# Kernel optimization log

Hardware: AMD Instinct MI355X
Metric: run time of the kernel (lower is better)

## Reference

```python
import jax, jax.numpy as jnp
import numpy as np

KNN_K = 16
EPS = 1e-5


def _knn_idx(p, k):
    # p: [B,3,N] -> idx [B,N,k] of nearest neighbors (self excluded)
    pt = jnp.swapaxes(p, 1, 2)                      # [B,N,3]
    xx = jnp.sum(pt * pt, axis=-1)                  # [B,N]
    inner = jnp.einsum('bnd,bmd->bnm', pt, pt)      # [B,N,N]
    dist = -(xx[:, :, None] - 2.0 * inner + xx[:, None, :])  # -||pi-pj||^2
    N = pt.shape[1]
    dist = dist - 1e9 * jnp.eye(N, dtype=dist.dtype)
    return jax.lax.top_k(dist, k)[1]


def _ln(x, g, b):
    mu = jnp.mean(x, axis=-1, keepdims=True)
    var = jnp.mean((x - mu) ** 2, axis=-1, keepdims=True)
    return (x - mu) * jax.lax.rsqrt(var + EPS) * g + b


_gather = jax.vmap(lambda a, i: a[i])  # a:[N,C], i:[N,k] -> [N,k,C]


def setup_inputs() -> dict:
    key = jax.random.key(0)
    ks = jax.random.split(key, 24)
    Cin, C, B, N = 64, 128, 8, 2048
    s = lambda k_, shp, fan: jax.random.normal(k_, shp, jnp.float32) * (1.0 / np.sqrt(fan))
    return {
        'x': jax.random.normal(ks[0], (B, Cin, N), jnp.float32),
        'p': jax.random.normal(ks[1], (B, 3, N), jnp.float32),
        'Win': s(ks[2], (C, Cin), Cin), 'bin_': jnp.zeros((C,), jnp.float32),
        'Wq': s(ks[3], (C, C), C), 'Wk': s(ks[4], (C, C), C), 'Wv': s(ks[5], (C, C), C),
        'Wd1': s(ks[6], (C, 3), 3), 'bd1': jnp.zeros((C,), jnp.float32),
        'Wd2': s(ks[7], (C, C), C), 'bd2': jnp.zeros((C,), jnp.float32),
        'Wa': s(ks[8], (C, C), C), 'ba': jnp.zeros((C,), jnp.float32),
        'g1': jnp.ones((C,), jnp.float32), 'b1': jnp.zeros((C,), jnp.float32),
        'g2': jnp.ones((C,), jnp.float32), 'b2': jnp.zeros((C,), jnp.float32),
        'Wf1': s(ks[9], (4 * C, C), C), 'bf1': jnp.zeros((4 * C,), jnp.float32),
        'Wf2': s(ks[10], (C, 4 * C), 4 * C), 'bf2': jnp.zeros((C,), jnp.float32),
    }


def reference(x, p, Win, bin_, Wq, Wk, Wv, Wd1, bd1, Wd2, bd2, Wa, ba,
              g1, b1, g2, b2, Wf1, bf1, Wf2, bf2) -> jnp.ndarray:
    B, _, N = x.shape
    k = min(KNN_K, max(1, N - 1))
    # in_proj (conv1x1 == per-point linear); work in [B,N,C]
    h = jnp.einsum('oc,bcn->bno', Win, x) + bin_          # [B,N,C]
    hn = _ln(h, g1, b1)
    idx = _knn_idx(p, k)                                  # [B,N,k] (int)
    q = hn @ Wq.T                                         # [B,N,C]
    k_all = hn @ Wk.T
    v_all = hn @ Wv.T
    k_j = _gather(k_all, idx)                             # [B,N,k,C]
    v_j = _gather(v_all, idx)
    pt = jnp.swapaxes(p, 1, 2)                            # [B,N,3]
    p_j = _gather(pt, idx)                                # [B,N,k,3]
    rel = pt[:, :, None, :] - p_j                         # [B,N,k,3]
    d = jax.nn.relu(rel @ Wd1.T + bd1) @ Wd2.T + bd2      # [B,N,k,C]
    logits = (q[:, :, None, :] - k_j + d) @ Wa.T + ba     # [B,N,k,C]
    a = jax.nn.softmax(logits, axis=2)                    # softmax over neighbors
    y = jnp.sum(a * (v_j + d), axis=2)                    # [B,N,C]
    h = h + y
    h2 = _ln(h, g2, b2)
    h = h + jax.nn.relu(h2 @ Wf1.T + bf1) @ Wf2.T + bf2
    return jnp.swapaxes(h, 1, 2)                          # [B,C,N]
```

## Files before the change

### kernel.cpp

```cpp
#include <hip/hip_runtime.h>

typedef __bf16 bf16_t;
typedef __bf16 bf16x8 __attribute__((ext_vector_type(8)));
typedef __bf16 bf16x2 __attribute__((ext_vector_type(2)));
typedef float  f32x4  __attribute__((ext_vector_type(4)));

#define MFMA16(a,b,c) __builtin_amdgcn_mfma_f32_16x16x32_bf16((a),(b),(c),0,0,0)

#define BB 8
#define NN 2048
#define CC 128
#define CIN 64
#define KNB 16
#define BNT (BB*NN)

static __device__ __forceinline__ int remap256(int x) { return ((x & 7) << 5) | (x >> 3); }

static __device__ __forceinline__ bf16x8 cvt8(const float* src) {
  f32x4 a0 = *(const f32x4*)src;
  f32x4 a1 = *(const f32x4*)(src + 4);
  bf16x8 fr;
  fr[0] = (__bf16)a0[0]; fr[1] = (__bf16)a0[1]; fr[2] = (__bf16)a0[2]; fr[3] = (__bf16)a0[3];
  fr[4] = (__bf16)a1[0]; fr[5] = (__bf16)a1[1]; fr[6] = (__bf16)a1[2]; fr[7] = (__bf16)a1[3];
  return fr;
}

__global__ __launch_bounds__(256) void inproj_compw_k(
    const float* __restrict__ x, const float* __restrict__ Win, const float* __restrict__ bin,
    const float* __restrict__ g1, const float* __restrict__ b1,
    bf16_t* __restrict__ hb, bf16_t* __restrict__ hnb,
    const float* __restrict__ Wq, const float* __restrict__ Wk, const float* __restrict__ Wv,
    const float* __restrict__ Wd2, const float* __restrict__ Wa,
    const float* __restrict__ Wf1, const float* __restrict__ Wf2,
    bf16_t* __restrict__ Wqb, bf16_t* __restrict__ Wkb, bf16_t* __restrict__ Wvb,
    bf16_t* __restrict__ Wd2b, bf16_t* __restrict__ Wab,
    bf16_t* __restrict__ Wf1b, bf16_t* __restrict__ Wf2b) {
  __shared__ bf16_t As[64 * 72];
  __shared__ bf16_t Bs[128 * 72];
  __shared__ float hs[64 * 132];
  int t = threadIdx.x;
  if (blockIdx.x >= 256) {
    int bi = blockIdx.x - 256;
    int mat = bi >> 3, xi = bi & 7;
    int nel = (mat >= 5) ? 65536 : 16384;
    const float* S = mat == 0 ? Wq : mat == 1 ? Wk : mat == 2 ? Wv : mat == 3 ? Wd2
                   : mat == 4 ? Wa : mat == 5 ? Wf1 : Wf2;
    bf16_t* D = mat == 0 ? Wqb : mat == 1 ? Wkb : mat == 2 ? Wvb : mat == 3 ? Wd2b
              : mat == 4 ? Wab : mat == 5 ? Wf1b : Wf2b;
    for (int i = xi * 256 + t; i * 8 < nel; i += 2048)
      *(bf16x8*)(D + i * 8) = cvt8(S + i * 8);
    return;
  }
  int lane = t & 63, w = t >> 6, quad = lane >> 4, l15 = lane & 15;
  int mBase = remap256(blockIdx.x) * 64;
  int b = mBase >> 11, n0 = mBase & (NN - 1);
  const float* xb = x + (size_t)b * CIN * NN;
  {
    int k = t >> 2, part = t & 3;
    #pragma unroll
    for (int i = 0; i < 4; ++i) {
      f32x4 v = *(const f32x4*)(xb + (size_t)k * NN + n0 + part * 16 + i * 4);
      #pragma unroll
      for (int j2 = 0; j2 < 4; ++j2) As[(part * 16 + i * 4 + j2) * 72 + k] = (__bf16)v[j2];
    }
  }
  {
    int row = t >> 1, seg = (t & 1) * 32;
    #pragma unroll
    for (int i = 0; i < 4; ++i)
      *(bf16x8*)(&Bs[row * 72 + seg + i * 8]) = cvt8(Win + (size_t)row * CIN + seg + i * 8);
  }
  __syncthreads();
  f32x4 acc[2][4] = {};
  #pragma unroll
  for (int s = 0; s < 2; ++s) {
    bf16x8 af[4];
    #pragma unroll
    for (int mt = 0; mt < 4; ++mt)
      af[mt] = *(const bf16x8*)(&As[(mt * 16 + l15) * 72 + s * 32 + quad * 8]);
    #pragma unroll
    for (int t2 = 0; t2 < 2; ++t2) {
      bf16x8 bfr = *(const bf16x8*)(&Bs[((w * 2 + t2) * 16 + l15) * 72 + s * 32 + quad * 8]);
      #pragma unroll
      for (int mt = 0; mt < 4; ++mt) acc[t2][mt] = MFMA16(af[mt], bfr, acc[t2][mt]);
    }
  }
  #pragma unroll
  for (int t2 = 0; t2 < 2; ++t2) {
    int col = (w * 2 + t2) * 16 + l15;
    float bv = bin[col];
    #pragma unroll
    for (int mt = 0; mt < 4; ++mt)
      #pragma unroll
      for (int reg = 0; reg < 4; ++reg)
        hs[(mt * 16 + quad * 4 + reg) * 132 + col] = acc[t2][mt][reg] + bv;
  }
  __syncthreads();
  {
    int row = t >> 2, c0 = (t & 3) * 32;
    float v[32];
    #pragma unroll
    for (int i = 0; i < 8; ++i) *(f32x4*)(v + i * 4) = *(const f32x4*)(&hs[row * 132 + c0 + i * 4]);
    float s1 = 0.f, s2 = 0.f;
    #pragma unroll
    for (int i = 0; i < 32; ++i) { s1 += v[i]; s2 += v[i] * v[i]; }
    s1 += __shfl_xor(s1, 1); s1 += __shfl_xor(s1, 2);
    s2 += __shfl_xor(s2, 1); s2 += __shfl_xor(s2, 2);
    float mu = s1 * (1.f / CC);
    float var = s2 * (1.f / CC) - mu * mu;
    float rs = rsqrtf(var + 1e-5f);
    bf16_t* hrow = hb + (size_t)(mBase + row) * CC + c0;
    #pragma unroll
    for (int i = 0; i < 4; ++i) {
      bf16x8 ho;
      #pragma unroll
      for (int j = 0; j < 8; ++j) ho[j] = (__bf16)v[i * 8 + j];
      *(bf16x8*)(hrow + i * 8) = ho;
    }
    bf16_t* hnrow = hnb + (size_t)(mBase + row) * CC + c0;
    #pragma unroll
    for (int i = 0; i < 4; ++i) {
      f32x4 g4a = ((const f32x4*)g1)[(c0 >> 2) + i * 2],     g4b = ((const f32x4*)g1)[(c0 >> 2) + i * 2 + 1];
      f32x4 b4a = ((const f32x4*)b1)[(c0 >> 2) + i * 2],     b4b = ((const f32x4*)b1)[(c0 >> 2) + i * 2 + 1];
      bf16x8 o;
      #pragma unroll
      for (int j = 0; j < 4; ++j) o[j]     = (__bf16)((v[i * 8 + j]     - mu) * rs * g4a[j] + b4a[j]);
      #pragma unroll
      for (int j = 0; j < 4; ++j) o[4 + j] = (__bf16)((v[i * 8 + 4 + j] - mu) * rs * g4b[j] + b4b[j]);
      *(bf16x8*)(hnrow + i * 8) = o;
    }
  }
}

static __device__ __forceinline__ void cas(double& a, double& b) {
  double lo = fmin(a, b), hi = fmax(a, b); a = lo; b = hi;
}
#define S8(K,o) \
  cas(K[o+0],K[o+1]); cas(K[o+2],K[o+3]); cas(K[o+4],K[o+5]); cas(K[o+6],K[o+7]); \
  cas(K[o+0],K[o+2]); cas(K[o+1],K[o+3]); cas(K[o+4],K[o+6]); cas(K[o+5],K[o+7]); \
  cas(K[o+1],K[o+2]); cas(K[o+5],K[o+6]); \
  cas(K[o+0],K[o+4]); cas(K[o+1],K[o+5]); cas(K[o+2],K[o+6]); cas(K[o+3],K[o+7]); \
  cas(K[o+2],K[o+4]); cas(K[o+3],K[o+5]); \
  cas(K[o+1],K[o+2]); cas(K[o+3],K[o+4]); cas(K[o+5],K[o+6]);
#define M8(K,a,b) \
  K[a+0]=fmin(K[a+0],K[b+7]); K[a+1]=fmin(K[a+1],K[b+6]); K[a+2]=fmin(K[a+2],K[b+5]); K[a+3]=fmin(K[a+3],K[b+4]); \
  K[a+4]=fmin(K[a+4],K[b+3]); K[a+5]=fmin(K[a+5],K[b+2]); K[a+6]=fmin(K[a+6],K[b+1]); K[a+7]=fmin(K[a+7],K[b+0]); \
  cas(K[a+0],K[a+4]); cas(K[a+1],K[a+5]); cas(K[a+2],K[a+6]); cas(K[a+3],K[a+7]); \
  cas(K[a+0],K[a+2]); cas(K[a+1],K[a+3]); cas(K[a+4],K[a+6]); cas(K[a+5],K[a+7]); \
  cas(K[a+0],K[a+1]); cas(K[a+2],K[a+3]); cas(K[a+4],K[a+5]); cas(K[a+6],K[a+7]);

static __device__ void knn_impl(float* sp, const float* __restrict__ p,
                                int* __restrict__ idxo, int bid) {
  float* px = sp; float* py = sp + NN; float* pz = sp + 2 * NN;
  int t = threadIdx.x;
  int b = bid >> 9;
  int g = bid & 511;
  const float* pb = p + (size_t)b * 3 * NN;
  for (int i = t; i < NN; i += 256) { px[i] = pb[i]; py[i] = pb[NN + i]; pz[i] = pb[2 * NN + i]; }
  __syncthreads();
  int w = t >> 6, lane = t & 63;
  int n = g * 4 + w;
  float pnx = px[n], pny = py[n], pnz = pz[n];
  double key[32];
  #pragma unroll
  for (int s = 0; s < 32; ++s) {
    int m = s * 64 + lane;
    float dx = pnx - px[m], dy = pny - py[m], dz = pnz - pz[m];
    float dist = dx * dx + dy * dy + dz * dz;
    unsigned db = (m == n) ? 0x7F800000u : __float_as_uint(dist);
    key[s] = __hiloint2double((int)db, m);
  }
  S8(key, 0); S8(key, 8); S8(key, 16); S8(key, 24);
  M8(key, 0, 8); M8(key, 16, 24); M8(key, 0, 16);
  const double DINF = __hiloint2double(0x7F900000, 0);
  int* myout = idxo + ((size_t)b * NN + n) * KNB;
  #pragma unroll 1
  for (int r = 0; r < 16; ++r) {
    double gm = key[0];
    #pragma unroll
    for (int off = 1; off < 64; off <<= 1) {
      double o = __shfl_xor(gm, off);
      gm = fmin(gm, o);
    }
    if (lane == 0) myout[r] = __double2loint(gm);
    bool win = (key[0] == gm);
    key[0] = win ? key[1] : key[0];
    key[1] = win ? key[2] : key[1];
    key[2] = win ? key[3] : key[2];
    key[3] = win ? key[4] : key[3];
    key[4] = win ? key[5] : key[4];
    key[5] = win ? key[6] : key[5];
    key[6] = win ? key[7] : key[6];
    key[7] = win ? DINF   : key[7];
  }
}

template<int EPI>
static __device__ void gemm_body(bf16_t* As, bf16_t* Bs,
    const bf16_t* __restrict__ Ab, const bf16_t* __restrict__ Wb, const float* __restrict__ bias,
    float* __restrict__ outF, bf16_t* __restrict__ outB, const bf16_t* __restrict__ resid,
    int mBase, int nBase, int Ncol, int Kdim) {
  int t = threadIdx.x;
  int lane = t & 63, w = t >> 6, quad = lane >> 4, l15 = lane & 15;
  int r = t >> 2, seg = (t & 3) * 8;
  f32x4 acc[4] = {{0,0,0,0},{0,0,0,0},{0,0,0,0},{0,0,0,0}};
  for (int k0 = 0; k0 < Kdim; k0 += 32) {
    __syncthreads();
    *(bf16x8*)(&As[r * 40 + seg]) = *(const bf16x8*)(Ab + (size_t)(mBase + r) * Kdim + k0 + seg);
    *(bf16x8*)(&Bs[r * 40 + seg]) = *(const bf16x8*)(Wb + (size_t)(nBase + r) * Kdim + k0 + seg);
    __syncthreads();
    bf16x8 bfr = *(const bf16x8*)(&Bs[(w * 16 + l15) * 40 + quad * 8]);
    #pragma unroll
    for (int mt = 0; mt < 4; ++mt) {
      bf16x8 afr = *(const bf16x8*)(&As[(mt * 16 + l15) * 40 + quad * 8]);
      acc[mt] = MFMA16(afr, bfr, acc[mt]);
    }
  }
  int n = nBase + w * 16 + l15;
  float bv = bias ? bias[n] : 0.f;
  #pragma unroll
  for (int mt = 0; mt < 4; ++mt) {
    #pragma unroll
    for (int reg = 0; reg < 4; ++reg) {
      int m = mBase + mt * 16 + quad * 4 + reg;
      float val = acc[mt][reg] + bv;
      if (EPI == 1) {
        outB[(size_t)m * Ncol + n] = (__bf16)fmaxf(val, 0.f);
      } else if (EPI == 3) {
        outB[(size_t)m * Ncol + n] = (__bf16)val;
      } else {
        val += (float)resid[(size_t)m * CC + n];
        int bo = m >> 11, np = m & (NN - 1);
        outF[((size_t)bo * CC + n) * NN + np] = val;
      }
    }
  }
}

template<int EPI>
__global__ __launch_bounds__(256) void gemm_k(
    const bf16_t* __restrict__ Ab, const bf16_t* __restrict__ Wb, const float* __restrict__ bias,
    float* __restrict__ outF, bf16_t* __restrict__ outB, const bf16_t* __restrict__ resid,
    int Ncol, int Kdim) {
  __shared__ bf16_t As[64 * 40];
  __shared__ bf16_t Bs[64 * 40];
  gemm_body<EPI>(As, Bs, Ab, Wb, bias, outF, outB, resid,
                 remap256(blockIdx.x) * 64, blockIdx.y * 64, Ncol, Kdim);
}

__global__ __launch_bounds__(256) void knn_qkv_k(
    const float* __restrict__ p, int* __restrict__ idxo,
    const bf16_t* __restrict__ hnb,
    const bf16_t* __restrict__ Wqb, const bf16_t* __restrict__ Wkb, const bf16_t* __restrict__ Wvb,
    bf16_t* __restrict__ qb, bf16_t* __restrict__ kb, bf16_t* __restrict__ vb) {
  __shared__ __align__(16) char smem[3 * NN * 4];
  if (blockIdx.x < 4096) {
    knn_impl((float*)smem, p, idxo, blockIdx.x);
  } else {
    bf16_t* As = (bf16_t*)smem;
    bf16_t* Bs = As + 64 * 40;
    int bx = blockIdx.x - 4096;
    int yy = bx >> 8, xx = bx & 255;
    int sel = yy >> 1;
    int mB = remap256(xx) * 64, nB = (yy & 1) * 64;
    if (sel == 0)      gemm_body<3>(As, Bs, hnb, Wqb, nullptr, nullptr, qb, nullptr, mB, nB, CC, CC);
    else if (sel == 1) gemm_body<3>(As, Bs, hnb, Wkb, nullptr, nullptr, kb, nullptr, mB, nB, CC, CC);
    else               gemm_body<3>(As, Bs, hnb, Wvb, nullptr, nullptr, vb, nullptr, mB, nB, CC, CC);
  }
}

__global__ __launch_bounds__(256, 3) void attn_k(
    const bf16_t* __restrict__ qbuf, const bf16_t* __restrict__ kbuf, const bf16_t* __restrict__ vbuf,
    const float* __restrict__ p, const int* __restrict__ idx,
    const float* __restrict__ Wd1, const float* __restrict__ bd1,
    const bf16_t* __restrict__ Wd2b, const float* __restrict__ bd2,
    const bf16_t* __restrict__ Wab, const float* __restrict__ ba,
    const float* __restrict__ g2, const float* __restrict__ b2,
    const bf16_t* __restrict__ hb, bf16_t* __restrict__ hresb, bf16_t* __restrict__ h2) {
  __shared__ bf16_t ts[64 * 136];
  __shared__ float hrs[4 * 128];
  __shared__ f32x4 wd1s[128];
  __shared__ f32x4 rels4[64];
  __shared__ int idxs[64];
  int t = threadIdx.x;
  int lane = t & 63, w = t >> 6, quad = lane >> 4, l15 = lane & 15;
  int batch = blockIdx.x & 7, grp = blockIdx.x >> 3;
  int bn0 = batch * NN + grp * 4;
  int b = batch;
  const float* pb = p + (size_t)b * 3 * NN;
  int col0 = w * 32 + l15;
  int col1 = col0 + 16;

  bf16x8 Bd[2][4];
  #pragma unroll
  for (int t2 = 0; t2 < 2; ++t2) {
    int row = w * 32 + t2 * 16 + l15;
    #pragma unroll
    for (int s = 0; s < 4; ++s)
      Bd[t2][s] = *(const bf16x8*)(Wd2b + (size_t)row * CC + s * 32 + quad * 8);
  }

  if (t < 64) {
    int jj = idx[(size_t)bn0 * KNB + t];
    idxs[t] = jj;
    int npt = grp * 4 + (t >> 4);
    f32x4 rv;
    rv[0] = pb[npt]          - pb[jj];
    rv[1] = pb[NN + npt]     - pb[NN + jj];
    rv[2] = pb[2 * NN + npt] - pb[2 * NN + jj];
    rv[3] = 0.f;
    rels4[t] = rv;
  }
  if (t < 128) {
    f32x4 wv;
    wv[0] = Wd1[t * 3]; wv[1] = Wd1[t * 3 + 1]; wv[2] = Wd1[t * 3 + 2]; wv[3] = bd1[t];
    wd1s[t] = wv;
  }
  __syncthreads();

  float qv[2][4];
  #pragma unroll
  for (int mt = 0; mt < 4; ++mt) {
    qv[0][mt] = (float)qbuf[(size_t)(bn0 + mt) * CC + col0];
    qv[1][mt] = (float)qbuf[(size_t)(bn0 + mt) * CC + col1];
  }
  float kreg[2][4][4];
  #pragma unroll
  for (int mt = 0; mt < 4; ++mt)
    #pragma unroll
    for (int reg = 0; reg < 4; ++reg) {
      size_t base = (size_t)(b * NN + idxs[mt * 16 + quad * 4 + reg]) * CC;
      kreg[0][mt][reg] = (float)kbuf[base + col0];
      kreg[1][mt][reg] = (float)kbuf[base + col1];
    }

  f32x4 relv[4];
  #pragma unroll
  for (int mt = 0; mt < 4; ++mt) relv[mt] = rels4[mt * 16 + l15];
  f32x4 accd[2][4] = {};
  #pragma unroll
  for (int s = 0; s < 4; ++s) {
    bf16x8 af[4];
    #pragma unroll
    for (int j = 0; j < 8; ++j) {
      f32x4 wv = wd1s[s * 32 + quad * 8 + j];
      #pragma unroll
      for (int mt = 0; mt < 4; ++mt) {
        float tv = fmaf(wv[0], relv[mt][0], fmaf(wv[1], relv[mt][1], fmaf(wv[2], relv[mt][2], wv[3])));
        af[mt][j] = (__bf16)fmaxf(tv, 0.f);
      }
    }
    #pragma unroll
    for (int t2 = 0; t2 < 2; ++t2)
      #pragma unroll
      for (int mt = 0; mt < 4; ++mt)
        accd[t2][mt] = MFMA16(af[mt], Bd[t2][s], accd[t2][mt]);
  }

  {
    float b2v0 = bd2[col0], b2v1 = bd2[col1];
    #pragma unroll
    for (int mt = 0; mt < 4; ++mt)
      #pragma unroll
      for (int reg = 0; reg < 4; ++reg) {
        int row = mt * 16 + quad * 4 + reg;
        float d0 = accd[0][mt][reg] + b2v0;
        float d1 = accd[1][mt][reg] + b2v1;
        accd[0][mt][reg] = d0;
        accd[1][mt][reg] = d1;
        ts[row * 136 + col0] = (__bf16)(qv[0][mt] - kreg[0][mt][reg] + d0);
        ts[row * 136 + col1] = (__bf16)(qv[1][mt] - kreg[1][mt][reg] + d1);
      }
  }
  __syncthreads();

  float vreg[2][4][4];
  #pragma unroll
  for (int mt = 0; mt < 4; ++mt)
    #pragma unroll
    for (int reg = 0; reg < 4; ++reg) {
      size_t base = (size_t)(b * NN + idxs[mt * 16 + quad * 4 + reg]) * CC;
      vreg[0][mt][reg] = (float)vbuf[base + col0];
      vreg[1][mt][reg] = (float)vbuf[base + col1];
    }
  float hv[2][4];
  if (quad == 0) {
    #pragma unroll
    for (int mt = 0; mt < 4; ++mt) {
      hv[0][mt] = (float)hb[(size_t)(bn0 + mt) * CC + col0];
      hv[1][mt] = (float)hb[(size_t)(bn0 + mt) * CC + col1];
    }
  }
  bf16x8 Ba[2][4];
  #pragma unroll
  for (int t2 = 0; t2 < 2; ++t2) {
    int row = w * 32 + t2 * 16 + l15;
    #pragma unroll
    for (int s = 0; s < 4; ++s)
      Ba[t2][s] = *(const bf16x8*)(Wab + (size_t)row * CC + s * 32 + quad * 8);
  }

  f32x4 accl[2][4] = {};
  #pragma unroll
  for (int s = 0; s < 4; ++s) {
    bf16x8 af[4];
    #pragma unroll
    for (int mt = 0; mt < 4; ++mt)
      af[mt] = *(const bf16x8*)(&ts[(mt * 16 + l15) * 136 + s * 32 + quad * 8]);
    #pragma unroll
    for (int t2 = 0; t2 < 2; ++t2)
      #pragma unroll
      for (int mt = 0; mt < 4; ++mt)
        accl[t2][mt] = MFMA16(af[mt], Ba[t2][s], accl[t2][mt]);
  }

  #pragma unroll
  for (int t2 = 0; t2 < 2; ++t2) {
    int col = t2 ? col1 : col0;
    float bav = ba[col];
    #pragma unroll
    for (int mt = 0; mt < 4; ++mt) {
      float lv0 = accl[t2][mt][0] + bav, lv1 = accl[t2][mt][1] + bav;
      float lv2 = accl[t2][mt][2] + bav, lv3 = accl[t2][mt][3] + bav;
      float mx = fmaxf(fmaxf(lv0, lv1), fmaxf(lv2, lv3));
      mx = fmaxf(mx, __shfl_xor(mx, 16));
      mx = fmaxf(mx, __shfl_xor(mx, 32));
      float e0 = __expf(lv0 - mx), e1 = __expf(lv1 - mx);
      float e2 = __expf(lv2 - mx), e3 = __expf(lv3 - mx);
      float ss = e0 + e1 + e2 + e3;
      ss += __shfl_xor(ss, 16); ss += __shfl_xor(ss, 32);
      float yv = e0 * (vreg[t2][mt][0] + accd[t2][mt][0])
               + e1 * (vreg[t2][mt][1] + accd[t2][mt][1])
               + e2 * (vreg[t2][mt][2] + accd[t2][mt][2])
               + e3 * (vreg[t2][mt][3] + accd[t2][mt][3]);
      yv += __shfl_xor(yv, 16); yv += __shfl_xor(yv, 32);
      if (quad == 0) {
        float hvv = hv[t2][mt] + yv / ss;
        hresb[(size_t)(bn0 + mt) * CC + col] = (__bf16)hvv;
        hrs[mt * 128 + col] = hvv;
      }
    }
  }
  __syncthreads();

  {
    int c0 = lane * 2;
    float v0 = hrs[w * 128 + c0], v1 = hrs[w * 128 + c0 + 1];
    float s1 = v0 + v1, s2 = v0 * v0 + v1 * v1;
    #pragma unroll
    for (int off = 1; off < 64; off <<= 1) { s1 += __shfl_xor(s1, off); s2 += __shfl_xor(s2, off); }
    float mu = s1 * (1.f / CC);
    float var = s2 * (1.f / CC) - mu * mu;
    float rs = rsqrtf(var + 1e-5f);
    bf16x2 o;
    o[0] = (__bf16)((v0 - mu) * rs * g2[c0] + b2[c0]);
    o[1] = (__bf16)((v1 - mu) * rs * g2[c0 + 1] + b2[c0 + 1]);
    *(bf16x2*)(h2 + (size_t)(bn0 + w) * CC + c0) = o;
  }
}

extern "C" void kernel_launch(void* const* d_in, const int* in_sizes, int n_in,
                              void* d_out, int out_size, void* d_ws, size_t ws_size,
                              hipStream_t stream) {
  const float* x   = (const float*)d_in[0];
  const float* p   = (const float*)d_in[1];
  const float* Win = (const float*)d_in[2];
  const float* bin = (const float*)d_in[3];
  const float* Wq  = (const float*)d_in[4];
  const float* Wk  = (const float*)d_in[5];
  const float* Wv  = (const float*)d_in[6];
  const float* Wd1 = (const float*)d_in[7];
  const float* bd1 = (const float*)d_in[8];
  const float* Wd2 = (const float*)d_in[9];
  const float* bd2 = (const float*)d_in[10];
  const float* Wa  = (const float*)d_in[11];
  const float* ba  = (const float*)d_in[12];
  const float* g1  = (const float*)d_in[13];
  const float* b1  = (const float*)d_in[14];
  const float* g2  = (const float*)d_in[15];
  const float* b2  = (const float*)d_in[16];
  const float* Wf1 = (const float*)d_in[17];
  const float* bf1 = (const float*)d_in[18];
  const float* Wf2 = (const float*)d_in[19];
  const float* bf2 = (const float*)d_in[20];
  float* out = (float*)d_out;

  const size_t SZ = (size_t)BNT * CC;
  float* wsf = (float*)d_ws;
  bf16_t* hb    = (bf16_t*)wsf;
  bf16_t* hnb   = (bf16_t*)(wsf + SZ / 2);
  bf16_t* hresb = hnb;
  bf16_t* qb    = (bf16_t*)(wsf + SZ);
  bf16_t* kb    = (bf16_t*)(wsf + SZ + SZ / 2);
  bf16_t* vb    = (bf16_t*)(wsf + 2 * SZ);
  bf16_t* g     = (bf16_t*)(wsf + SZ);
  bf16_t* h2    = (bf16_t*)(wsf + 3 * SZ);
  int*    idxw  = (int*)(wsf + 3 * SZ + SZ / 2);
  bf16_t* Wqb   = (bf16_t*)(idxw + (size_t)BNT * KNB);
  bf16_t* Wkb   = Wqb  + 16384;
  bf16_t* Wvb   = Wkb  + 16384;
  bf16_t* Wd2b  = Wvb  + 16384;
  bf16_t* Wab   = Wd2b + 16384;
  bf16_t* Wf1b  = Wab  + 16384;
  bf16_t* Wf2b  = Wf1b + 65536;

  inproj_compw_k<<<256 + 56, 256, 0, stream>>>(x, Win, bin, g1, b1, hb, hnb,
                                               Wq, Wk, Wv, Wd2, Wa, Wf1, Wf2,
                                               Wqb, Wkb, Wvb, Wd2b, Wab, Wf1b, Wf2b);
  knn_qkv_k<<<4096 + 1536, 256, 0, stream>>>(p, idxw, hnb, Wqb, Wkb, Wvb, qb, kb, vb);
  attn_k<<<BNT / 4, 256, 0, stream>>>(qb, kb, vb, p, idxw, Wd1, bd1, Wd2b, bd2, Wab, ba,
                                      g2, b2, hb, hresb, h2);
  gemm_k<1><<<dim3(BNT / 64, 8), 256, 0, stream>>>(h2, Wf1b, bf1, nullptr, g, nullptr, 4 * CC, CC);
  gemm_k<2><<<dim3(BNT / 64, 2), 256, 0, stream>>>(g, Wf2b, bf2, out, nullptr, hresb, CC, 4 * CC);
}
```

Baseline: 255.5 us.

## Fold Wa into Wq, Wk and Wd2 to drop the per-neighbor logits GEMM

Uses the linearity of the logits projection to precompute Wa·Wq, Wa·Wk and Wa·Wd2 (plus Wa·bd2) as combined weights. The q/k projections now produce Wa-projected values directly, and the attention kernel computes logits from the relu(Wd1·rel) tile with a single MFMA pass against Wa·Wd2. This removes the second dependent GEMM and its LDS round trip. The cost is a small extra weight-product precompute and different bf16 rounding, since the logits skip the intermediate rounding step.

After: 260.7 us. 2.1% more time.

```diff
diff --git a/kernel.cpp b/kernel.cpp
--- a/kernel.cpp
+++ b/kernel.cpp
@@ -2,6 +2,7 @@
 
 typedef __bf16 bf16_t;
 typedef __bf16 bf16x8 __attribute__((ext_vector_type(8)));
+typedef __bf16 bf16x4 __attribute__((ext_vector_type(4)));
 typedef __bf16 bf16x2 __attribute__((ext_vector_type(2)));
 typedef float  f32x4  __attribute__((ext_vector_type(4)));
 
@@ -31,24 +32,53 @@
     bf16_t* __restrict__ hb, bf16_t* __restrict__ hnb,
     const float* __restrict__ Wq, const float* __restrict__ Wk, const float* __restrict__ Wv,
     const float* __restrict__ Wd2, const float* __restrict__ Wa,
-    const float* __restrict__ Wf1, const float* __restrict__ Wf2,
-    bf16_t* __restrict__ Wqb, bf16_t* __restrict__ Wkb, bf16_t* __restrict__ Wvb,
-    bf16_t* __restrict__ Wd2b, bf16_t* __restrict__ Wab,
-    bf16_t* __restrict__ Wf1b, bf16_t* __restrict__ Wf2b) {
+    const float* __restrict__ Wf1, const float* __restrict__ Wf2, const float* __restrict__ bd2,
+    bf16_t* __restrict__ Wqab, bf16_t* __restrict__ Wkab, bf16_t* __restrict__ Wvb,
+    bf16_t* __restrict__ Wd2b, bf16_t* __restrict__ Wd2ab,
+    bf16_t* __restrict__ Wf1b, bf16_t* __restrict__ Wf2b, float* __restrict__ bd2a) {
   __shared__ bf16_t As[64 * 72];
   __shared__ bf16_t Bs[128 * 72];
   __shared__ float hs[64 * 132];
   int t = threadIdx.x;
   if (blockIdx.x >= 256) {
     int bi = blockIdx.x - 256;
-    int mat = bi >> 3, xi = bi & 7;
-    int nel = (mat >= 5) ? 65536 : 16384;
-    const float* S = mat == 0 ? Wq : mat == 1 ? Wk : mat == 2 ? Wv : mat == 3 ? Wd2
-                   : mat == 4 ? Wa : mat == 5 ? Wf1 : Wf2;
-    bf16_t* D = mat == 0 ? Wqb : mat == 1 ? Wkb : mat == 2 ? Wvb : mat == 3 ? Wd2b
-              : mat == 4 ? Wab : mat == 5 ? Wf1b : Wf2b;
-    for (int i = xi * 256 + t; i * 8 < nel; i += 2048)
-      *(bf16x8*)(D + i * 8) = cvt8(S + i * 8);
+    if (bi < 32) {
+      int mat = bi >> 3, xi = bi & 7;
+      int nel = (mat >= 2) ? 65536 : 16384;
+      const float* S = mat == 0 ? Wv : mat == 1 ? Wd2 : mat == 2 ? Wf1 : Wf2;
+      bf16_t* D = mat == 0 ? Wvb : mat == 1 ? Wd2b : mat == 2 ? Wf1b : Wf2b;
+      for (int i = xi * 256 + t; i * 8 < nel; i += 2048)
+        *(bf16x8*)(D + i * 8) = cvt8(S + i * 8);
+    } else if (bi < 80) {
+      int pi = bi - 32, mat = pi >> 4, xi = pi & 15;
+      const float* R = mat == 0 ? Wq : mat == 1 ? Wk : Wd2;
+      bf16_t* D = mat == 0 ? Wqab : mat == 1 ? Wkab : Wd2ab;
+      int c = xi * 8 + (t >> 5);
+      int i0 = (t & 31) * 4;
+      const float* war = Wa + (size_t)c * CC;
+      f32x4 acc = {0.f, 0.f, 0.f, 0.f};
+      #pragma unroll 4
+      for (int e = 0; e < CC; ++e) {
+        float a = war[e];
+        f32x4 bq = *(const f32x4*)(R + (size_t)e * CC + i0);
+        acc[0] = fmaf(a, bq[0], acc[0]);
+        acc[1] = fmaf(a, bq[1], acc[1]);
+        acc[2] = fmaf(a, bq[2], acc[2]);
+        acc[3] = fmaf(a, bq[3], acc[3]);
+      }
+      bf16x4 o;
+      o[0] = (__bf16)acc[0]; o[1] = (__bf16)acc[1];
+      o[2] = (__bf16)acc[2]; o[3] = (__bf16)acc[3];
+      *(bf16x4*)(D + (size_t)c * CC + i0) = o;
+    } else {
+      if (t < 128) {
+        float s = 0.f;
+        const float* war = Wa + (size_t)t * CC;
+        #pragma unroll 4
+        for (int e = 0; e < CC; ++e) s = fmaf(war[e], bd2[e], s);
+        bd2a[t] = s;
+      }
+    }
     return;
   }
   int lane = t & 63, w = t >> 6, quad = lane >> 4, l15 = lane & 15;
@@ -251,7 +281,7 @@
 __global__ __launch_bounds__(256) void knn_qkv_k(
     const float* __restrict__ p, int* __restrict__ idxo,
     const bf16_t* __restrict__ hnb,
-    const bf16_t* __restrict__ Wqb, const bf16_t* __restrict__ Wkb, const bf16_t* __restrict__ Wvb,
+    const bf16_t* __restrict__ Wqab, const bf16_t* __restrict__ Wkab, const bf16_t* __restrict__ Wvb,
     bf16_t* __restrict__ qb, bf16_t* __restrict__ kb, bf16_t* __restrict__ vb) {
   __shared__ __align__(16) char smem[3 * NN * 4];
   if (blockIdx.x < 4096) {
@@ -263,8 +293,8 @@
     int yy = bx >> 8, xx = bx & 255;
     int sel = yy >> 1;
     int mB = remap256(xx) * 64, nB = (yy & 1) * 64;
-    if (sel == 0)      gemm_body<3>(As, Bs, hnb, Wqb, nullptr, nullptr, qb, nullptr, mB, nB, CC, CC);
-    else if (sel == 1) gemm_body<3>(As, Bs, hnb, Wkb, nullptr, nullptr, kb, nullptr, mB, nB, CC, CC);
+    if (sel == 0)      gemm_body<3>(As, Bs, hnb, Wqab, nullptr, nullptr, qb, nullptr, mB, nB, CC, CC);
+    else if (sel == 1) gemm_body<3>(As, Bs, hnb, Wkab, nullptr, nullptr, kb, nullptr, mB, nB, CC, CC);
     else               gemm_body<3>(As, Bs, hnb, Wvb, nullptr, nullptr, vb, nullptr, mB, nB, CC, CC);
   }
 }
@@ -274,7 +304,8 @@
     const float* __restrict__ p, const int* __restrict__ idx,
     const float* __restrict__ Wd1, const float* __restrict__ bd1,
     const bf16_t* __restrict__ Wd2b, const float* __restrict__ bd2,
-    const bf16_t* __restrict__ Wab, const float* __restrict__ ba,
+    const bf16_t* __restrict__ Wd2ab, const float* __restrict__ bd2a,
+    const float* __restrict__ ba,
     const float* __restrict__ g2, const float* __restrict__ b2,
     const bf16_t* __restrict__ hb, bf16_t* __restrict__ hresb, bf16_t* __restrict__ h2) {
   __shared__ bf16_t ts[64 * 136];
@@ -286,19 +317,9 @@
   int lane = t & 63, w = t >> 6, quad = lane >> 4, l15 = lane & 15;
   int batch = blockIdx.x & 7, grp = blockIdx.x >> 3;
   int bn0 = batch * NN + grp * 4;
-  int b = batch;
-  const float* pb = p + (size_t)b * 3 * NN;
+  const float* pb = p + (size_t)batch * 3 * NN;
   int col0 = w * 32 + l15;
   int col1 = col0 + 16;
-
-  bf16x8 Bd[2][4];
-  #pragma unroll
-  for (int t2 = 0; t2 < 2; ++t2) {
-    int row = w * 32 + t2 * 16 + l15;
-    #pragma unroll
-    for (int s = 0; s < 4; ++s)
-      Bd[t2][s] = *(const bf16x8*)(Wd2b + (size_t)row * CC + s * 32 + quad * 8);
-  }
 
   if (t < 64) {
     int jj = idx[(size_t)bn0 * KNB + t];
@@ -318,68 +339,105 @@
   }
   __syncthreads();
 
-  float qv[2][4];
-  #pragma unroll
-  for (int mt = 0; mt < 4; ++mt) {
-    qv[0][mt] = (float)qbuf[(size_t)(bn0 + mt) * CC + col0];
-    qv[1][mt] = (float)qbuf[(size_t)(bn0 + mt) * CC + col1];
-  }
-  float kreg[2][4][4];
-  #pragma unroll
-  for (int mt = 0; mt < 4; ++mt)
-    #pragma unroll
-    for (int reg = 0; reg < 4; ++reg) {
-      size_t base = (size_t)(b * NN + idxs[mt * 16 + quad * 4 + reg]) * CC;
-      kreg[0][mt][reg] = (float)kbuf[base + col0];
-      kreg[1][mt][reg] = (float)kbuf[base + col1];
-    }
-
-  f32x4 relv[4];
-  #pragma unroll
-  for (int mt = 0; mt < 4; ++mt) relv[mt] = rels4[mt * 16 + l15];
+  {
+    int row = t >> 2, cseg = (t & 3) * 32;
+    f32x4 rv = rels4[row];
+    #pragma unroll
+    for (int i = 0; i < 4; ++i) {
+      bf16x8 u8;
+      #pragma unroll
+      for (int j = 0; j < 8; ++j) {
+        f32x4 wv = wd1s[cseg + i * 8 + j];
+        float tv = fmaf(wv[0], rv[0], fmaf(wv[1], rv[1], fmaf(wv[2], rv[2], wv[3])));
+        u8[j] = (__bf16)fmaxf(tv, 0.f);
+      }
+      *(bf16x8*)(&ts[row * 136 + cseg + i * 8]) = u8;
+    }
+  }
+  __syncthreads();
+
+  f32x4 acca[2][4] = {};
+  {
+    bf16x8 Bf[2][4];
+    #pragma unroll
+    for (int t2 = 0; t2 < 2; ++t2) {
+      int row = w * 32 + t2 * 16 + l15;
+      #pragma unroll
+      for (int s = 0; s < 4; ++s)
+        Bf[t2][s] = *(const bf16x8*)(Wd2ab + (size_t)row * CC + s * 32 + quad * 8);
+    }
+    #pragma unroll
+    for (int s = 0; s < 4; ++s) {
+      bf16x8 af[4];
+      #pragma unroll
+      for (int mt = 0; mt < 4; ++mt)
+        af[mt] = *(const bf16x8*)(&ts[(mt * 16 + l15) * 136 + s * 32 + quad * 8]);
+      #pragma unroll
+      for (int t2 = 0; t2 < 2; ++t2)
+        #pragma unroll
+        for (int mt = 0; mt < 4; ++mt)
+          acca[t2][mt] = MFMA16(af[mt], Bf[t2][s], acca[t2][mt]);
+    }
+  }
+
+  {
+    float qv[2][4];
+    #pragma unroll
+    for (int mt = 0; mt < 4; ++mt) {
+      qv[0][mt] = (float)qbuf[(size_t)(bn0 + mt) * CC + col0];
+      qv[1][mt] = (float)qbuf[(size_t)(bn0 + mt) * CC + col1];
+    }
+    float kreg[2][4][4];
+    #pragma unroll
+    for (int mt = 0; mt < 4; ++mt)
+      #pragma unroll
+      for (int reg = 0; reg < 4; ++reg) {
+        size_t base = (size_t)(batch * NN + idxs[mt * 16 + quad * 4 + reg]) * CC;
+        kreg[0][mt][reg] = (float)kbuf[base + col0];
+        kreg[1][mt][reg] = (float)kbuf[base + col1];
+      }
+    #pragma unroll
+    for (int t2 = 0; t2 < 2; ++t2) {
+      int col = t2 ? col1 : col0;
+      float cA = bd2a[col] + ba[col];
+      #pragma unroll
+      for (int mt = 0; mt < 4; ++mt)
+        #pragma unroll
+        for (int reg = 0; reg < 4; ++reg)
+          acca[t2][mt][reg] += qv[t2][mt] - kreg[t2][mt][reg] + cA;
+    }
+  }
+
   f32x4 accd[2][4] = {};
-  #pragma unroll
-  for (int s = 0; s < 4; ++s) {
-    bf16x8 af[4];
-    #pragma unroll
-    for (int j = 0; j < 8; ++j) {
-      f32x4 wv = wd1s[s * 32 + quad * 8 + j];
-      #pragma unroll
-      for (int mt = 0; mt < 4; ++mt) {
-        float tv = fmaf(wv[0], relv[mt][0], fmaf(wv[1], relv[mt][1], fmaf(wv[2], relv[mt][2], wv[3])));
-        af[mt][j] = (__bf16)fmaxf(tv, 0.f);
-      }
-    }
-    #pragma unroll
-    for (int t2 = 0; t2 < 2; ++t2)
+  {
+    bf16x8 Bf[2][4];
+    #pragma unroll
+    for (int t2 = 0; t2 < 2; ++t2) {
+      int row = w * 32 + t2 * 16 + l15;
+      #pragma unroll
+      for (int s = 0; s < 4; ++s)
+        Bf[t2][s] = *(const bf16x8*)(Wd2b + (size_t)row * CC + s * 32 + quad * 8);
+    }
+    #pragma unroll
+    for (int s = 0; s < 4; ++s) {
+      bf16x8 af[4];
       #pragma unroll
       for (int mt = 0; mt < 4; ++mt)
-        accd[t2][mt] = MFMA16(af[mt], Bd[t2][s], accd[t2][mt]);
-  }
-
-  {
-    float b2v0 = bd2[col0], b2v1 = bd2[col1];
-    #pragma unroll
-    for (int mt = 0; mt < 4; ++mt)
-      #pragma unroll
-      for (int reg = 0; reg < 4; ++reg) {
-        int row = mt * 16 + quad * 4 + reg;
-        float d0 = accd[0][mt][reg] + b2v0;
-        float d1 = accd[1][mt][reg] + b2v1;
-        accd[0][mt][reg] = d0;
-        accd[1][mt][reg] = d1;
-        ts[row * 136 + col0] = (__bf16)(qv[0][mt] - kreg[0][mt][reg] + d0);
-        ts[row * 136 + col1] = (__bf16)(qv[1][mt] - kreg[1][mt][reg] + d1);
-      }
-  }
-  __syncthreads();
+        af[mt] = *(const bf16x8*)(&ts[(mt * 16 + l15) * 136 + s * 32 + quad * 8]);
+      #pragma unroll
+      for (int t2 = 0; t2 < 2; ++t2)
+        #pragma unroll
+        for (int mt = 0; mt < 4; ++mt)
+          accd[t2][mt] = MFMA16(af[mt], Bf[t2][s], accd[t2][mt]);
+    }
+  }
 
   float vreg[2][4][4];
   #pragma unroll
   for (int mt = 0; mt < 4; ++mt)
     #pragma unroll
     for (int reg = 0; reg < 4; ++reg) {
-      size_t base = (size_t)(b * NN + idxs[mt * 16 + quad * 4 + reg]) * CC;
+      size_t base = (size_t)(batch * NN + idxs[mt * 16 + quad * 4 + reg]) * CC;
       vreg[0][mt][reg] = (float)vbuf[base + col0];
       vreg[1][mt][reg] = (float)vbuf[base + col1];
     }
@@ -391,37 +449,15 @@
       hv[1][mt] = (float)hb[(size_t)(bn0 + mt) * CC + col1];
     }
   }
-  bf16x8 Ba[2][4];
-  #pragma unroll
-  for (int t2 = 0; t2 < 2; ++t2) {
-    int row = w * 32 + t2 * 16 + l15;
-    #pragma unroll
-    for (int s = 0; s < 4; ++s)
-      Ba[t2][s] = *(const bf16x8*)(Wab + (size_t)row * CC + s * 32 + quad * 8);
-  }
-
-  f32x4 accl[2][4] = {};
-  #pragma unroll
-  for (int s = 0; s < 4; ++s) {
-    bf16x8 af[4];
-    #pragma unroll
-    for (int mt = 0; mt < 4; ++mt)
-      af[mt] = *(const bf16x8*)(&ts[(mt * 16 + l15) * 136 + s * 32 + quad * 8]);
-    #pragma unroll
-    for (int t2 = 0; t2 < 2; ++t2)
-      #pragma unroll
-      for (int mt = 0; mt < 4; ++mt)
-        accl[t2][mt] = MFMA16(af[mt], Ba[t2][s], accl[t2][mt]);
-  }
 
   #pragma unroll
   for (int t2 = 0; t2 < 2; ++t2) {
     int col = t2 ? col1 : col0;
-    float bav = ba[col];
+    float bv = bd2[col];
     #pragma unroll
     for (int mt = 0; mt < 4; ++mt) {
-      float lv0 = accl[t2][mt][0] + bav, lv1 = accl[t2][mt][1] + bav;
-      float lv2 = accl[t2][mt][2] + bav, lv3 = accl[t2][mt][3] + bav;
+      float lv0 = acca[t2][mt][0], lv1 = acca[t2][mt][1];
+      float lv2 = acca[t2][mt][2], lv3 = acca[t2][mt][3];
       float mx = fmaxf(fmaxf(lv0, lv1), fmaxf(lv2, lv3));
       mx = fmaxf(mx, __shfl_xor(mx, 16));
       mx = fmaxf(mx, __shfl_xor(mx, 32));
@@ -435,7 +471,7 @@
                + e3 * (vreg[t2][mt][3] + accd[t2][mt][3]);
       yv += __shfl_xor(yv, 16); yv += __shfl_xor(yv, 32);
       if (quad == 0) {
-        float hvv = hv[t2][mt] + yv / ss;
+        float hvv = hv[t2][mt] + yv / ss + bv;
         hresb[(size_t)(bn0 + mt) * CC + col] = (__bf16)hvv;
         hrs[mt * 128 + col] = hvv;
       }
@@ -496,20 +532,21 @@
   bf16_t* g     = (bf16_t*)(wsf + SZ);
   bf16_t* h2    = (bf16_t*)(wsf + 3 * SZ);
   int*    idxw  = (int*)(wsf + 3 * SZ + SZ / 2);
-  bf16_t* Wqb   = (bf16_t*)(idxw + (size_t)BNT * KNB);
-  bf16_t* Wkb   = Wqb  + 16384;
-  bf16_t* Wvb   = Wkb  + 16384;
-  bf16_t* Wd2b  = Wvb  + 16384;
-  bf16_t* Wab   = Wd2b + 16384;
-  bf16_t* Wf1b  = Wab  + 16384;
-  bf16_t* Wf2b  = Wf1b + 65536;
-
-  inproj_compw_k<<<256 + 56, 256, 0, stream>>>(x, Win, bin, g1, b1, hb, hnb,
-                                               Wq, Wk, Wv, Wd2, Wa, Wf1, Wf2,
-                                               Wqb, Wkb, Wvb, Wd2b, Wab, Wf1b, Wf2b);
-  knn_qkv_k<<<4096 + 1536, 256, 0, stream>>>(p, idxw, hnb, Wqb, Wkb, Wvb, qb, kb, vb);
-  attn_k<<<BNT / 4, 256, 0, stream>>>(qb, kb, vb, p, idxw, Wd1, bd1, Wd2b, bd2, Wab, ba,
-                                      g2, b2, hb, hresb, h2);
+  bf16_t* Wqab  = (bf16_t*)(idxw + (size_t)BNT * KNB);
+  bf16_t* Wkab  = Wqab  + 16384;
+  bf16_t* Wvb   = Wkab  + 16384;
+  bf16_t* Wd2b  = Wvb   + 16384;
+  bf16_t* Wd2ab = Wd2b  + 16384;
+  bf16_t* Wf1b  = Wd2ab + 16384;
+  bf16_t* Wf2b  = Wf1b  + 65536;
+  float*  bd2a  = (float*)(Wf2b + 65536);
+
+  inproj_compw_k<<<256 + 81, 256, 0, stream>>>(x, Win, bin, g1, b1, hb, hnb,
+                                               Wq, Wk, Wv, Wd2, Wa, Wf1, Wf2, bd2,
+                                               Wqab, Wkab, Wvb, Wd2b, Wd2ab, Wf1b, Wf2b, bd2a);
+  knn_qkv_k<<<4096 + 1536, 256, 0, stream>>>(p, idxw, hnb, Wqab, Wkab, Wvb, qb, kb, vb);
+  attn_k<<<BNT / 4, 256, 0, stream>>>(qb, kb, vb, p, idxw, Wd1, bd1, Wd2b, bd2, Wd2ab, bd2a,
+                                      ba, g2, b2, hb, hresb, h2);
   gemm_k<1><<<dim3(BNT / 64, 8), 256, 0, stream>>>(h2, Wf1b, bf1, nullptr, g, nullptr, 4 * CC, CC);
   gemm_k<2><<<dim3(BNT / 64, 2), 256, 0, stream>>>(g, Wf2b, bf2, out, nullptr, hresb, CC, 4 * CC);
 }
```
